# Performance work log

Hardware: AMD Instinct MI355X
Metric: run time of the kernel (lower is better)

## Reference

```python
import jax, jax.numpy as jnp
import numpy as np

NUM_USERS = 100000
NUM_ITEMS = 50000
N_NODES = NUM_USERS + NUM_ITEMS
NUM_COMMUNITY = 64
N_LAYERS = 3
NNZ = 2400000
BATCH = 8192
NEG_SLOPE = 0.1
EPS = 1e-12


def setup_inputs() -> dict:
    key = jax.random.key(0)
    ks = jax.random.split(key, 9)
    stdv = 1.0 / np.sqrt(NUM_COMMUNITY)
    return {
        "users": jax.random.randint(ks[0], (BATCH,), 0, NUM_USERS, dtype=jnp.int64 if jax.config.jax_enable_x64 else jnp.int32).astype(jnp.int32),
        "adjacent_items": jax.random.randint(ks[1], (BATCH,), 0, NUM_ITEMS).astype(jnp.int32),
        "weak_items": jax.random.randint(ks[2], (BATCH,), 0, NUM_ITEMS).astype(jnp.int32),
        "strong_items": jax.random.randint(ks[3], (BATCH,), 0, NUM_ITEMS).astype(jnp.int32),
        "edge_rows": jax.random.randint(ks[4], (NNZ,), 0, N_NODES).astype(jnp.int32),
        "edge_cols": jax.random.randint(ks[5], (NNZ,), 0, N_NODES).astype(jnp.int32),
        "edge_vals": jax.random.uniform(ks[6], (NNZ,), dtype=jnp.float32),
        "user_preference": jax.random.uniform(ks[7], (NUM_USERS, NUM_COMMUNITY), dtype=jnp.float32, minval=-stdv, maxval=stdv),
        "item_preference": jax.random.uniform(ks[8], (NUM_ITEMS, NUM_COMMUNITY), dtype=jnp.float32, minval=-stdv, maxval=stdv),
    }


def _lrelu_l2norm(x):
    # leaky_relu(neg_slope=0.1) then L2-normalize along last dim (torch F.normalize semantics)
    x = jnp.where(x >= 0, x, NEG_SLOPE * x)
    norm = jnp.sqrt(jnp.sum(x * x, axis=-1, keepdims=True))
    return x / jnp.maximum(norm, EPS)


def reference(users, adjacent_items, weak_items, strong_items,
              edge_rows, edge_cols, edge_vals,
              user_preference, item_preference):
    # ---- computer(): LightGCN-style propagation over sparse adjacency ----
    pref = _lrelu_l2norm(jnp.concatenate([user_preference, item_preference], axis=0))  # [N, C]
    acc = pref
    p = pref
    for _ in range(N_LAYERS):
        # sparse.mm(Graph, p): gather source rows, scale by edge values, scatter-add into dest rows
        msg = edge_vals[:, None] * p[edge_cols]                      # [nnz, C]
        p = jax.ops.segment_sum(msg, edge_rows, num_segments=N_NODES)  # [N, C]
        p = _lrelu_l2norm(p)
        acc = acc + p
    merged = acc / (N_LAYERS + 1)  # mean over stacked layers
    users_pref = merged[:NUM_USERS]
    items_pref = merged[NUM_USERS:]

    # ---- forward(): per-pair dot products + sigmoid ----
    u = users_pref[users]  # [B, C]

    def score(items):
        return jax.nn.sigmoid(jnp.sum(u * items_pref[items], axis=-1))

    # stack of (adjacent, weak, strong) gamma preferences, shape [3, B]
    return jnp.stack([score(adjacent_items), score(weak_items), score(strong_items)], axis=0)
```

## Files before the change

### kernel.cpp

```cpp
#include <hip/hip_runtime.h>
#include <hip/hip_fp16.h>
#include <math.h>

#define D 64
#define NUM_USERS 100000
#define NUM_ITEMS 50000
#define N_NODES 150000
#define NNZ 2400000
#define BATCH 8192
#define NEG_SLOPE 0.1f
#define EPS_NRM 1e-12f

#define NB2     293
#define RPB     512
#define NCHUNK  256
#define CH      9376
#define NHT     (NB2 * NCHUNK)
#define NBH     (NHT / 256)
#define CAP     10240
#define VSCALE  16383.f

typedef unsigned short ushort_t;

__device__ __forceinline__ float wave_sum64(float v) {
    #pragma unroll
    for (int off = 32; off > 0; off >>= 1)
        v += __shfl_xor(v, off, 64);
    return v;
}

__device__ __forceinline__ int wave_sum64_i(int v) {
    #pragma unroll
    for (int off = 32; off > 0; off >>= 1)
        v += __shfl_xor(v, off, 64);
    return v;
}

__device__ __forceinline__ float h2f_lo(unsigned u) {
    return __half2float(__ushort_as_half((unsigned short)(u & 0xFFFFu)));
}
__device__ __forceinline__ float h2f_hi(unsigned u) {
    return __half2float(__ushort_as_half((unsigned short)(u >> 16)));
}


__global__ void __launch_bounds__(512) bucket_hist(const int* __restrict__ rows,
                                                   int* __restrict__ ht) {
    __shared__ int hist[NB2];
    int c = blockIdx.x, tid = threadIdx.x;
    for (int b = tid; b < NB2; b += 512) hist[b] = 0;
    __syncthreads();
    int base = c * CH;
    int n = NNZ - base; if (n > CH) n = CH;
    const int4* r4 = (const int4*)(rows + base);
    for (int i = tid; i < (n >> 2); i += 512) {
        int4 r = r4[i];
        atomicAdd(&hist[r.x >> 9], 1);
        atomicAdd(&hist[r.y >> 9], 1);
        atomicAdd(&hist[r.z >> 9], 1);
        atomicAdd(&hist[r.w >> 9], 1);
    }
    __syncthreads();
    for (int b = tid; b < NB2; b += 512) ht[b * NCHUNK + c] = hist[b];
}

__global__ void scan1_kernel(const int* __restrict__ in, int* __restrict__ out,
                             int* __restrict__ bsums, int n) {
    int tid = threadIdx.x, gid = blockIdx.x * 256 + tid;
    int v = (gid < n) ? in[gid] : 0;
    int lane = tid & 63, w = tid >> 6;
    int s = v;
    #pragma unroll
    for (int off = 1; off < 64; off <<= 1) {
        int t = __shfl_up(s, off, 64);
        if (lane >= off) s += t;
    }
    __shared__ int wsum[4];
    if (lane == 63) wsum[w] = s;
    __syncthreads();
    if (tid == 0) {
        int a = 0;
        #pragma unroll
        for (int i = 0; i < 4; i++) { int t = wsum[i]; wsum[i] = a; a += t; }
    }
    __syncthreads();
    int incl = s + wsum[w];
    if (gid < n) out[gid] = incl - v;
    if (tid == 255) bsums[blockIdx.x] = incl;
}

__global__ void scan3_kernel(int* __restrict__ out, const int* __restrict__ bsums, int n) {
    __shared__ int wtot[4];
    __shared__ int total;
    int b = blockIdx.x, tid = threadIdx.x;
    int lane = tid & 63, w = tid >> 6;
    int partial = 0;
    for (int i = tid; i < b; i += 256) partial += bsums[i];
    partial = wave_sum64_i(partial);
    if (lane == 0) wtot[w] = partial;
    __syncthreads();
    if (tid == 0) total = wtot[0] + wtot[1] + wtot[2] + wtot[3];
    __syncthreads();
    int gid = b * 256 + tid;
    if (gid < n) out[gid] += total;
}

__global__ void __launch_bounds__(1024) bucket_scatter(
        const int* __restrict__ rows, const int* __restrict__ cols,
        const float* __restrict__ vals, const int* __restrict__ hoff,
        unsigned* __restrict__ es4, ushort_t* __restrict__ rlow) {
    __shared__ int cur[NB2];
    int c = blockIdx.x, tid = threadIdx.x;
    if (tid < NB2) cur[tid] = hoff[tid * NCHUNK + c];
    __syncthreads();
    int base = c * CH;
    int n = NNZ - base; if (n > CH) n = CH;
    const int4*   r4 = (const int4*)(rows + base);
    const int4*   c4 = (const int4*)(cols + base);
    const float4* v4 = (const float4*)(vals + base);
    for (int i = tid; i < (n >> 2); i += 1024) {
        int4 r = r4[i];
        int4 cc = c4[i];
        float4 v = v4[i];
        int p;
        p = atomicAdd(&cur[r.x >> 9], 1);
        es4[p] = (unsigned)cc.x | ((unsigned)(v.x * VSCALE + 0.5f) << 18);
        rlow[p] = (ushort_t)(r.x & (RPB - 1));
        p = atomicAdd(&cur[r.y >> 9], 1);
        es4[p] = (unsigned)cc.y | ((unsigned)(v.y * VSCALE + 0.5f) << 18);
        rlow[p] = (ushort_t)(r.y & (RPB - 1));
        p = atomicAdd(&cur[r.z >> 9], 1);
        es4[p] = (unsigned)cc.z | ((unsigned)(v.z * VSCALE + 0.5f) << 18);
        rlow[p] = (ushort_t)(r.z & (RPB - 1));
        p = atomicAdd(&cur[r.w >> 9], 1);
        es4[p] = (unsigned)cc.w | ((unsigned)(v.w * VSCALE + 0.5f) << 18);
        rlow[p] = (ushort_t)(r.w & (RPB - 1));
    }
}

__global__ void __launch_bounds__(1024) bucket_sort(const unsigned* __restrict__ es4,
                                                    const ushort_t* __restrict__ rlow,
                                                    const int* __restrict__ hoff,
                                                    unsigned* __restrict__ es,
                                                    int* __restrict__ rowptr) {
    __shared__ int      hist[RPB];
    __shared__ int      wsum[8];
    __shared__ unsigned outbuf[CAP];
    int b = blockIdx.x, tid = threadIdx.x;
    int beg = hoff[b * NCHUNK];
    int end = (b == NB2 - 1) ? NNZ : hoff[(b + 1) * NCHUNK];
    if (tid < RPB) hist[tid] = 0;
    __syncthreads();
    for (int i = beg + tid; i < end; i += 1024)
        atomicAdd(&hist[rlow[i]], 1);
    __syncthreads();
    int excl = 0;
    if (tid < RPB) {
        int v = hist[tid];
        int lane = tid & 63, w = tid >> 6;
        int s = v;
        #pragma unroll
        for (int off = 1; off < 64; off <<= 1) {
            int t = __shfl_up(s, off, 64);
            if (lane >= off) s += t;
        }
        if (lane == 63) wsum[w] = s;
        excl = s - v;
    }
    __syncthreads();
    if (tid == 0) {
        int a = 0;
        #pragma unroll
        for (int i = 0; i < 8; i++) { int t = wsum[i]; wsum[i] = a; a += t; }
    }
    __syncthreads();
    if (tid < RPB) {
        excl += wsum[tid >> 6];
        int r = b * RPB + tid;
        if (r <= N_NODES) rowptr[r] = beg + excl;
        hist[tid] = excl;
    }
    __syncthreads();
    for (int i = beg + tid; i < end; i += 1024) {
        int d = atomicAdd(&hist[rlow[i]], 1);
        outbuf[d] = es4[i];
    }
    __syncthreads();
    int n = end - beg;
    for (int i = tid; i < n; i += 1024)
        es[beg + i] = outbuf[i];
}

__global__ void init_kernel(const float* __restrict__ upref,
                            const float* __restrict__ ipref,
                            __half* __restrict__ p0) {
    int row  = blockIdx.x * 4 + (threadIdx.x >> 6);
    int lane = threadIdx.x & 63;
    if (row >= N_NODES) return;
    float x = (row < NUM_USERS) ? upref[(size_t)row * D + lane]
                                : ipref[(size_t)(row - NUM_USERS) * D + lane];
    x = (x >= 0.f) ? x : NEG_SLOPE * x;
    float norm = sqrtf(wave_sum64(x * x));
    float y = x / fmaxf(norm, EPS_NRM);
    p0[(size_t)row * D + lane] = __float2half(y);
}

__device__ __forceinline__ void acc8(float a[8], float v, uint4 q) {
    a[0] = fmaf(v, h2f_lo(q.x), a[0]);
    a[1] = fmaf(v, h2f_hi(q.x), a[1]);
    a[2] = fmaf(v, h2f_lo(q.y), a[2]);
    a[3] = fmaf(v, h2f_hi(q.y), a[3]);
    a[4] = fmaf(v, h2f_lo(q.z), a[4]);
    a[5] = fmaf(v, h2f_hi(q.z), a[5]);
    a[6] = fmaf(v, h2f_lo(q.w), a[6]);
    a[7] = fmaf(v, h2f_hi(q.w), a[7]);
}

__global__ void gather_kernel(const int* __restrict__ rowptr,
                              const unsigned* __restrict__ es,
                              const __half* __restrict__ p,
                              __half* __restrict__ pn) {
    int tid  = threadIdx.x;
    int row  = blockIdx.x * 8 + (tid >> 5);
    if (row >= N_NODES) return;
    int hl   = tid & 31;
    int sub  = hl >> 3;
    int fl   = hl & 7;
    int beg = rowptr[row], end = rowptr[row + 1];

    float a[8];
    #pragma unroll
    for (int k = 0; k < 8; k++) a[k] = 0.f;

    const float vs = 1.f / VSCALE;
    int e = beg + sub;
    while (e + 4 < end) {
        unsigned ev0 = es[e];
        unsigned ev1 = es[e + 4];
        const uint4 q0 = *(const uint4*)(p + (((ev0 & 0x3FFFFu) << 6) | (fl << 3)));
        const uint4 q1 = *(const uint4*)(p + (((ev1 & 0x3FFFFu) << 6) | (fl << 3)));
        float v0 = (float)(ev0 >> 18) * vs;
        float v1 = (float)(ev1 >> 18) * vs;
        acc8(a, v0, q0);
        acc8(a, v1, q1);
        e += 8;
    }
    if (e < end) {
        unsigned ev = es[e];
        const uint4 q = *(const uint4*)(p + (((ev & 0x3FFFFu) << 6) | (fl << 3)));
        float v = (float)(ev >> 18) * vs;
        acc8(a, v, q);
    }

    bool s0 = (sub & 1) != 0, s1 = (sub & 2) != 0;
    float b1[4];
    #pragma unroll
    for (int j = 0; j < 4; j++) {
        int c4 = (j >> 1) * 4, bb = j & 1;
        float keep = s0 ? a[c4 + 2 + bb] : a[c4 + bb];
        float send = s0 ? a[c4 + bb]     : a[c4 + 2 + bb];
        b1[j] = keep + __shfl_xor(send, 8, 64);
    }
    float cf[2];
    #pragma unroll
    for (int bb = 0; bb < 2; bb++) {
        float keep = s1 ? b1[2 + bb] : b1[bb];
        float send = s1 ? b1[bb]     : b1[2 + bb];
        cf[bb] = keep + __shfl_xor(send, 16, 64);
    }
    float y0 = (cf[0] >= 0.f) ? cf[0] : NEG_SLOPE * cf[0];
    float y1 = (cf[1] >= 0.f) ? cf[1] : NEG_SLOPE * cf[1];
    float ss = fmaf(y0, y0, y1 * y1);
    ss += __shfl_xor(ss, 16, 64);
    ss += __shfl_xor(ss, 8, 64);
    ss += __shfl_xor(ss, 4, 64);
    ss += __shfl_xor(ss, 2, 64);
    ss += __shfl_xor(ss, 1, 64);
    float inv = 1.f / fmaxf(sqrtf(ss), EPS_NRM);
    __half2 o = __floats2half2_rn(y0 * inv, y1 * inv);
    *(__half2*)(pn + (size_t)row * D + fl * 8 + 2 * sub) = o;
}

__global__ void score_kernel(const int* __restrict__ users,
                             const int* __restrict__ it0,
                             const int* __restrict__ it1,
                             const int* __restrict__ it2,
                             const __half* __restrict__ p0,
                             const __half* __restrict__ p1,
                             const __half* __restrict__ p2,
                             const __half* __restrict__ p3,
                             float* __restrict__ out) {
    int b    = blockIdx.x * 4 + (threadIdx.x >> 6);
    int lane = threadIdx.x & 63;
    if (b >= BATCH) return;
    int u = users[b];
    size_t uo = (size_t)u * D + lane;
    float uf = __half2float(p0[uo]) + __half2float(p1[uo])
             + __half2float(p2[uo]) + __half2float(p3[uo]);

    int its[3];
    its[0] = it0[b]; its[1] = it1[b]; its[2] = it2[b];
    #pragma unroll
    for (int k = 0; k < 3; k++) {
        size_t io = (size_t)(NUM_USERS + its[k]) * D + lane;
        float itf = __half2float(p0[io]) + __half2float(p1[io])
                  + __half2float(p2[io]) + __half2float(p3[io]);
        float s = wave_sum64(uf * itf) * 0.0625f;
        if (lane == 0)
            out[k * BATCH + b] = 1.f / (1.f + expf(-s));
    }
}

extern "C" void kernel_launch(void* const* d_in, const int* in_sizes, int n_in,
                              void* d_out, int out_size, void* d_ws, size_t ws_size,
                              hipStream_t stream) {
    const int*   users  = (const int*)  d_in[0];
    const int*   adj    = (const int*)  d_in[1];
    const int*   weak   = (const int*)  d_in[2];
    const int*   strong = (const int*)  d_in[3];
    const int*   erows  = (const int*)  d_in[4];
    const int*   ecols  = (const int*)  d_in[5];
    const float* evals  = (const float*)d_in[6];
    const float* upref  = (const float*)d_in[7];
    const float* ipref  = (const float*)d_in[8];
    float* out = (float*)d_out;

    const size_t rowElems = (size_t)N_NODES * D;

    char* base = (char*)d_ws;
    size_t off = 0;
    auto alloc = [&](size_t bytes) {
        char* p = base + off;
        off = (off + bytes + 255) & ~(size_t)255;
        return (void*)p;
    };
    __half*   p0     = (__half*)  alloc(rowElems * sizeof(__half));
    __half*   p1     = (__half*)  alloc(rowElems * sizeof(__half));
    __half*   p2     = (__half*)  alloc(rowElems * sizeof(__half));
    __half*   p3     = (__half*)  alloc(rowElems * sizeof(__half));
    unsigned* es     = (unsigned*)alloc((size_t)NNZ * sizeof(unsigned));
    int*      ht     = (int*)     alloc((size_t)NHT * sizeof(int));
    int*      hoff   = (int*)     alloc((size_t)NHT * sizeof(int));
    int*      rowptr = (int*)     alloc((N_NODES + 2) * sizeof(int));
    int*      bsums  = (int*)     alloc(1024 * sizeof(int));
    unsigned* es4t   = (unsigned*)p2;
    ushort_t* rlowt  = (ushort_t*)((char*)p2 + (size_t)NNZ * 4);

    bucket_hist   <<<NCHUNK, 512, 0, stream>>>(erows, ht);
    scan1_kernel  <<<NBH, 256, 0, stream>>>(ht, hoff, bsums, NHT);
    scan3_kernel  <<<NBH, 256, 0, stream>>>(hoff, bsums, NHT);
    bucket_scatter<<<NCHUNK, 1024, 0, stream>>>(erows, ecols, evals, hoff, es4t, rlowt);
    bucket_sort   <<<NB2, 1024, 0, stream>>>(es4t, rlowt, hoff, es, rowptr);

    init_kernel<<<(N_NODES + 3) / 4, 256, 0, stream>>>(upref, ipref, p0);
    gather_kernel<<<N_NODES / 8, 256, 0, stream>>>(rowptr, es, p0, p1);
    gather_kernel<<<N_NODES / 8, 256, 0, stream>>>(rowptr, es, p1, p2);
    gather_kernel<<<N_NODES / 8, 256, 0, stream>>>(rowptr, es, p2, p3);

    score_kernel<<<(BATCH + 3) / 4, 256, 0, stream>>>(users, adj, weak, strong,
                                                      p0, p1, p2, p3, out);
}
```

Before: 336.8 us.

## Fold histogram scan into scatter and sort kernels; unroll gather deeper

Removes the two standalone scan kernels. bucket_scatter now computes its per-bucket offsets by summing the histogram table directly, and bucket_sort computes its segment start and end by reducing prefixes of the table. Each block redoes part of the scan work, which is redundant, in exchange for two fewer launches and no intermediate offsets buffer. The gather loop also gains a 4-way unrolled body with more loads in flight and is given a launch_bounds occupancy hint.

```diff
diff --git a/kernel.cpp b/kernel.cpp
--- a/kernel.cpp
+++ b/kernel.cpp
@@ -16,7 +16,6 @@
 #define NCHUNK  256
 #define CH      9376
 #define NHT     (NB2 * NCHUNK)
-#define NBH     (NHT / 256)
 #define CAP     10240
 #define VSCALE  16383.f
 
@@ -64,55 +63,42 @@
     for (int b = tid; b < NB2; b += 512) ht[b * NCHUNK + c] = hist[b];
 }
 
-__global__ void scan1_kernel(const int* __restrict__ in, int* __restrict__ out,
-                             int* __restrict__ bsums, int n) {
-    int tid = threadIdx.x, gid = blockIdx.x * 256 + tid;
-    int v = (gid < n) ? in[gid] : 0;
+__global__ void __launch_bounds__(1024) bucket_scatter(
+        const int* __restrict__ rows, const int* __restrict__ cols,
+        const float* __restrict__ vals, const int* __restrict__ ht,
+        unsigned* __restrict__ es4, ushort_t* __restrict__ rlow) {
+    __shared__ int cur[NB2];
+    __shared__ int wsum[8];
+    int c = blockIdx.x, tid = threadIdx.x;
+    int tot = 0, part = 0;
+    if (tid < NB2) {
+        const int* rowp = ht + tid * NCHUNK;
+        for (int cc = 0; cc < c; cc++)  part += rowp[cc];
+        tot = part;
+        for (int cc = c; cc < NCHUNK; cc++) tot += rowp[cc];
+    }
     int lane = tid & 63, w = tid >> 6;
-    int s = v;
-    #pragma unroll
-    for (int off = 1; off < 64; off <<= 1) {
-        int t = __shfl_up(s, off, 64);
-        if (lane >= off) s += t;
-    }
-    __shared__ int wsum[4];
-    if (lane == 63) wsum[w] = s;
+    int excl = 0;
+    if (tid < 512) {
+        int s = tot;
+        #pragma unroll
+        for (int off = 1; off < 64; off <<= 1) {
+            int t = __shfl_up(s, off, 64);
+            if (lane >= off) s += t;
+        }
+        if (lane == 63) wsum[w] = s;
+        excl = s - tot;
+    }
     __syncthreads();
     if (tid == 0) {
         int a = 0;
         #pragma unroll
-        for (int i = 0; i < 4; i++) { int t = wsum[i]; wsum[i] = a; a += t; }
-    }
-    __syncthreads();
-    int incl = s + wsum[w];
-    if (gid < n) out[gid] = incl - v;
-    if (tid == 255) bsums[blockIdx.x] = incl;
-}
-
-__global__ void scan3_kernel(int* __restrict__ out, const int* __restrict__ bsums, int n) {
-    __shared__ int wtot[4];
-    __shared__ int total;
-    int b = blockIdx.x, tid = threadIdx.x;
-    int lane = tid & 63, w = tid >> 6;
-    int partial = 0;
-    for (int i = tid; i < b; i += 256) partial += bsums[i];
-    partial = wave_sum64_i(partial);
-    if (lane == 0) wtot[w] = partial;
-    __syncthreads();
-    if (tid == 0) total = wtot[0] + wtot[1] + wtot[2] + wtot[3];
-    __syncthreads();
-    int gid = b * 256 + tid;
-    if (gid < n) out[gid] += total;
-}
-
-__global__ void __launch_bounds__(1024) bucket_scatter(
-        const int* __restrict__ rows, const int* __restrict__ cols,
-        const float* __restrict__ vals, const int* __restrict__ hoff,
-        unsigned* __restrict__ es4, ushort_t* __restrict__ rlow) {
-    __shared__ int cur[NB2];
-    int c = blockIdx.x, tid = threadIdx.x;
-    if (tid < NB2) cur[tid] = hoff[tid * NCHUNK + c];
-    __syncthreads();
+        for (int i = 0; i < 8; i++) { int t = wsum[i]; wsum[i] = a; a += t; }
+    }
+    __syncthreads();
+    if (tid < NB2) cur[tid] = excl + wsum[w] + part;
+    __syncthreads();
+
     int base = c * CH;
     int n = NNZ - base; if (n > CH) n = CH;
     const int4*   r4 = (const int4*)(rows + base);
@@ -140,24 +126,41 @@
 
 __global__ void __launch_bounds__(1024) bucket_sort(const unsigned* __restrict__ es4,
                                                     const ushort_t* __restrict__ rlow,
-                                                    const int* __restrict__ hoff,
+                                                    const int* __restrict__ ht,
                                                     unsigned* __restrict__ es,
                                                     int* __restrict__ rowptr) {
     __shared__ int      hist[RPB];
-    __shared__ int      wsum[8];
+    __shared__ int      wsum[16];
+    __shared__ int      wsum2[16];
     __shared__ unsigned outbuf[CAP];
+    __shared__ int      sh_beg, sh_end;
     int b = blockIdx.x, tid = threadIdx.x;
-    int beg = hoff[b * NCHUNK];
-    int end = (b == NB2 - 1) ? NNZ : hoff[(b + 1) * NCHUNK];
+    int lane = tid & 63, w = tid >> 6;
+
+    int lim = b * NCHUNK;
+    int partial = 0;
+    for (int i = tid; i < lim; i += 1024) partial += ht[i];
+    int rpart = (tid < NCHUNK) ? ht[lim + tid] : 0;
+    partial = wave_sum64_i(partial);
+    rpart   = wave_sum64_i(rpart);
+    if (lane == 0) { wsum[w] = partial; wsum2[w] = rpart; }
+    __syncthreads();
+    if (tid == 0) {
+        int a = 0, r = 0;
+        #pragma unroll
+        for (int i = 0; i < 16; i++) { a += wsum[i]; r += wsum2[i]; }
+        sh_beg = a; sh_end = a + r;
+    }
     if (tid < RPB) hist[tid] = 0;
     __syncthreads();
+    int beg = sh_beg, end = sh_end;
+
     for (int i = beg + tid; i < end; i += 1024)
         atomicAdd(&hist[rlow[i]], 1);
     __syncthreads();
     int excl = 0;
     if (tid < RPB) {
         int v = hist[tid];
-        int lane = tid & 63, w = tid >> 6;
         int s = v;
         #pragma unroll
         for (int off = 1; off < 64; off <<= 1) {
@@ -216,7 +219,8 @@
     a[7] = fmaf(v, h2f_hi(q.w), a[7]);
 }
 
-__global__ void gather_kernel(const int* __restrict__ rowptr,
+__global__ void __launch_bounds__(256, 8) gather_kernel(
+                              const int* __restrict__ rowptr,
                               const unsigned* __restrict__ es,
                               const __half* __restrict__ p,
                               __half* __restrict__ pn) {
@@ -234,6 +238,25 @@
 
     const float vs = 1.f / VSCALE;
     int e = beg + sub;
+    while (e + 12 < end) {
+        unsigned ev0 = es[e];
+        unsigned ev1 = es[e + 4];
+        unsigned ev2 = es[e + 8];
+        unsigned ev3 = es[e + 12];
+        const uint4 q0 = *(const uint4*)(p + (((ev0 & 0x3FFFFu) << 6) | (fl << 3)));
+        const uint4 q1 = *(const uint4*)(p + (((ev1 & 0x3FFFFu) << 6) | (fl << 3)));
+        const uint4 q2 = *(const uint4*)(p + (((ev2 & 0x3FFFFu) << 6) | (fl << 3)));
+        const uint4 q3 = *(const uint4*)(p + (((ev3 & 0x3FFFFu) << 6) | (fl << 3)));
+        float v0 = (float)(ev0 >> 18) * vs;
+        float v1 = (float)(ev1 >> 18) * vs;
+        float v2 = (float)(ev2 >> 18) * vs;
+        float v3 = (float)(ev3 >> 18) * vs;
+        acc8(a, v0, q0);
+        acc8(a, v1, q1);
+        acc8(a, v2, q2);
+        acc8(a, v3, q3);
+        e += 16;
+    }
     while (e + 4 < end) {
         unsigned ev0 = es[e];
         unsigned ev1 = es[e + 4];
@@ -340,17 +363,13 @@
     __half*   p3     = (__half*)  alloc(rowElems * sizeof(__half));
     unsigned* es     = (unsigned*)alloc((size_t)NNZ * sizeof(unsigned));
     int*      ht     = (int*)     alloc((size_t)NHT * sizeof(int));
-    int*      hoff   = (int*)     alloc((size_t)NHT * sizeof(int));
     int*      rowptr = (int*)     alloc((N_NODES + 2) * sizeof(int));
-    int*      bsums  = (int*)     alloc(1024 * sizeof(int));
     unsigned* es4t   = (unsigned*)p2;
     ushort_t* rlowt  = (ushort_t*)((char*)p2 + (size_t)NNZ * 4);
 
     bucket_hist   <<<NCHUNK, 512, 0, stream>>>(erows, ht);
-    scan1_kernel  <<<NBH, 256, 0, stream>>>(ht, hoff, bsums, NHT);
-    scan3_kernel  <<<NBH, 256, 0, stream>>>(hoff, bsums, NHT);
-    bucket_scatter<<<NCHUNK, 1024, 0, stream>>>(erows, ecols, evals, hoff, es4t, rlowt);
-    bucket_sort   <<<NB2, 1024, 0, stream>>>(es4t, rlowt, hoff, es, rowptr);
+    bucket_scatter<<<NCHUNK, 1024, 0, stream>>>(erows, ecols, evals, ht, es4t, rlowt);
+    bucket_sort   <<<NB2, 1024, 0, stream>>>(es4t, rlowt, ht, es, rowptr);
 
     init_kernel<<<(N_NODES + 3) / 4, 256, 0, stream>>>(upref, ipref, p0);
     gather_kernel<<<N_NODES / 8, 256, 0, stream>>>(rowptr, es, p0, p1);
```

New measurement: 387.0 us. +14.9%, slower.
